# Kernel optimization log

Hardware: AMD Instinct MI355X
Metric: run time of the kernel (lower is better)

## Reference

```python
import jax, jax.numpy as jnp
import numpy as np

ALPHA, BETA, GAMMA = 1.0, 0.5, 0.25
FEATURE_DIM = 4
OHEM_RATIO = 3
K = 8  # fixed number of instance labels (0 = background)
DELTA_V, DELTA_D = 0.5, 1.5
EPS_DICE = 1e-3
EPS_IOU = 1e-6


def setup_inputs() -> dict:
    key = jax.random.key(0)
    k1, k2, k3, k4, k5 = jax.random.split(key, 5)
    B, h, w = 8, 160, 160
    H, W = 4 * h, 4 * w
    maps = jax.random.normal(k1, (B, 2 + FEATURE_DIM, h, w), jnp.float32)
    gt_texts = (jax.random.uniform(k2, (B, H, W)) > 0.5).astype(jnp.float32)
    gt_kernels = (jax.random.uniform(k3, (B, H, W)) > 0.6).astype(jnp.float32)
    training_masks = (jax.random.uniform(k4, (B, H, W)) > 0.05).astype(jnp.float32)
    gt_instance = jax.random.randint(k5, (B, H, W), 0, K).astype(jnp.int32)
    return dict(maps=maps, gt_texts=gt_texts, gt_kernels=gt_kernels,
                gt_instance=gt_instance, training_masks=training_masks)


def _up4(x):
    # F.interpolate(scale_factor=4, mode='nearest')
    return jnp.repeat(jnp.repeat(x, 4, axis=-2), 4, axis=-1)


def _dice(inp, tgt, mask):
    B = inp.shape[0]
    m = mask.reshape(B, -1)
    p = jax.nn.sigmoid(inp).reshape(B, -1) * m
    t = tgt.reshape(B, -1) * m
    a = jnp.sum(p * t, axis=1)
    b = jnp.sum(p * p, axis=1) + EPS_DICE
    c = jnp.sum(t * t, axis=1) + EPS_DICE
    return 1.0 - 2.0 * a / (b + c)  # [B]


def _ohem_single(score, gt, tm):
    pos = gt > 0.5
    pos_num = jnp.sum(pos) - jnp.sum(pos & (tm <= 0.5))
    neg = ~pos
    neg_num = jnp.minimum(pos_num * OHEM_RATIO, jnp.sum(neg))
    neg_scores = jnp.where(neg, score, -jnp.inf).ravel()
    sorted_desc = -jnp.sort(-neg_scores)
    idx = jnp.clip(neg_num - 1, 0, neg_scores.size - 1)
    thr = sorted_desc[idx]
    sel = (((score >= thr) | pos) & (tm > 0.5)).astype(tm.dtype)
    fallback = (pos_num == 0) | (neg_num == 0)
    return jnp.where(fallback, tm, sel)


def _emb_single(emb, instance, kernel, tm):
    # emb: [D,H,W]; EmbLoss v1 (agg/dis/reg), fixed K labels instead of torch.unique
    D = emb.shape[0]
    tm_b = tm > 0.5
    kn_b = kernel > 0.5
    inst = jnp.where(tm_b, instance, 0).ravel()              # instance * training_mask
    inst_k = jnp.where(kn_b & tm_b, instance, 0).ravel()     # instance * kernel
    e = emb.reshape(D, -1)                                   # [D,N]
    labels = jnp.arange(K)
    oh_k = (inst_k[None, :] == labels[:, None]).astype(e.dtype)   # [K,N]
    cnt_k = oh_k.sum(axis=1)                                  # [K]
    emb_mean = jnp.einsum('dn,kn->dk', e, oh_k) / jnp.maximum(cnt_k, 1.0)  # [D,K]
    nz = (labels != 0)
    emb_mean = emb_mean * nz[None, :].astype(e.dtype)          # torch skips lb==0 -> col0 stays 0
    present = cnt_k > 0
    valid = present & nz
    nv = jnp.sum(valid)

    # l_agg: per-pixel distance to own-instance mean
    mean_pix = emb_mean[:, inst]                               # [D,N]
    sqd = jnp.sum((e - mean_pix) ** 2, axis=0)
    dist = jnp.sqrt(jnp.maximum(sqd, 1e-12))
    val = jnp.log(jnp.maximum(dist - DELTA_V, 0.0) ** 2 + 1.0)
    oh_i = (inst[None, :] == labels[:, None]).astype(e.dtype)  # [K,N]
    cnt_i = oh_i.sum(axis=1)
    lagg_per = (oh_i @ val) / jnp.maximum(cnt_i, 1.0)          # [K]
    l_agg = jnp.sum(lagg_per * valid) / jnp.maximum(nv, 1)

    # l_dis: pairwise distances between instance means (off-diag, excl label 0)
    diff = emb_mean[:, :, None] - emb_mean[:, None, :]         # [D,K,K]
    sq = jnp.sum(diff ** 2, axis=0)
    pd = jnp.sqrt(jnp.where(sq > 0, sq, 1.0))                  # safe sqrt; diag masked below
    vdis = jnp.log(jnp.maximum(2.0 * DELTA_D - pd, 0.0) ** 2 + 1.0)
    pmask = (valid[:, None] & valid[None, :] & (~jnp.eye(K, dtype=bool))).astype(e.dtype)
    l_dis = jnp.sum(vdis * pmask) / jnp.maximum(pmask.sum(), 1.0)
    l_dis = jnp.where(nv >= 2, l_dis, 0.0)

    # l_reg over all present labels (col0 is zero -> contributes log(1)=0)
    num_instance = jnp.sum(present)
    l_reg = jnp.sum(jnp.log(jnp.linalg.norm(emb_mean, axis=0) + 1.0) * present) \
            / jnp.maximum(num_instance, 1) * 0.001

    loss = l_agg + l_dis + l_reg
    return jnp.where(nv > 0, loss, 0.0)


def reference(maps, gt_texts, gt_kernels, gt_instance, training_masks):
    p = _up4(maps)                     # [B,6,H,W]
    texts = p[:, 0]
    kernels = p[:, 1]
    embs = p[:, 2:]

    sel = jax.vmap(_ohem_single)(texts, gt_texts, training_masks)
    loss_text = _dice(texts, gt_texts, sel)

    sel_k = (jax.nn.sigmoid(texts) > 0.5).astype(texts.dtype) * training_masks
    loss_kernels = _dice(kernels, gt_kernels, sel_k)

    loss_emb = jax.vmap(_emb_single)(embs, gt_instance, gt_kernels, training_masks)

    loss = ALPHA * loss_text + BETA * loss_kernels + GAMMA * loss_emb  # [B]
    return jnp.mean(loss)  # reduction='mean'
```

## Files before the change

### kernel.cpp

```cpp
#include <hip/hip_runtime.h>
#include <math.h>

#define NB 8
#define CW 160
#define CPB (CW*CW)
#define FW 640
#define PIX (FW*FW)
#define MBLK 25

#define OFF_CNTS     0
#define OFF_CI       (NB*CPB*4)
#define OFF_CKC     (OFF_CI + NB*CPB*8)
#define OFF_PARTM   (OFF_CKC + NB*CPB*8)
#define OFF_PARTV   (OFF_PARTM + NB*MBLK*54*4)
#define WS_END      (OFF_PARTV + NB*MBLK*8*4)

__device__ __forceinline__ float wredf(float v) {
    #pragma unroll
    for (int o = 32; o; o >>= 1) v += __shfl_xor(v, o, 64);
    return v;
}
__device__ __forceinline__ int wredi(int v) {
    #pragma unroll
    for (int o = 32; o; o >>= 1) v += __shfl_xor(v, o, 64);
    return v;
}
__device__ __forceinline__ unsigned long long wredu64(unsigned long long v) {
    #pragma unroll
    for (int o = 32; o; o >>= 1) v += __shfl_xor(v, o, 64);
    return v;
}
__device__ __forceinline__ unsigned keyxf(float f) {
    unsigned bits = __float_as_uint(f);
    return (bits & 0x80000000u) ? ~bits : (bits | 0x80000000u);
}

__device__ int coscan(const int* hist, int nbins, int tid, int* s_sum) {
    int chunk = nbins >> 8;
    int base = tid * chunk;
    int s = 0;
    #pragma unroll 8
    for (int i = 0; i < chunk; i++) s += hist[base + i];
    s_sum[tid] = s;
    __syncthreads();
    #pragma unroll
    for (int off = 1; off < 256; off <<= 1) {
        int add = (tid >= off) ? s_sum[tid - off] : 0;
        __syncthreads();
        s_sum[tid] += add;
        __syncthreads();
    }
    return s_sum[255];
}
__device__ void cofind(const int* hist, int nbins, int tid,
                       const int* s_sum, int j, int* s_out) {
    int chunk = nbins >> 8;
    if (tid == 0) { s_out[0] = 0; s_out[1] = 0; }
    __syncthreads();
    int incl = s_sum[tid];
    int own = incl - ((tid > 0) ? s_sum[tid - 1] : 0);
    int excl = incl - own;
    if (j >= excl && j < incl) {
        int base = tid * chunk, cum = excl;
        for (int i = 0; i < chunk; i++) {
            int c = hist[base + i];
            if (j < cum + c) { s_out[0] = base + i; s_out[1] = j - cum; break; }
            cum += c;
        }
    }
    __syncthreads();
}
__device__ __forceinline__ int ohem_j(int pn, int N) {
    long long nn = min(3LL * (long long)pn, (long long)N);
    int j = (int)((long long)N - nn);
    if (j < 0) j = 0;
    if (j >= N) j = (N > 0) ? N - 1 : 0;
    return j;
}

__global__ __launch_bounds__(256) void k_pass1(const float* __restrict__ gt_texts,
                                               const float* __restrict__ gt_kernels,
                                               const int*   __restrict__ gt_instance,
                                               const float* __restrict__ tm,
                                               unsigned* __restrict__ cnts,
                                               unsigned long long* __restrict__ ciA,
                                               unsigned long long* __restrict__ ckA) {
    int b = blockIdx.x / 100;
    int cp = (blockIdx.x - b * 100) * 256 + threadIdx.x;
    int cy = cp / CW, cx = cp - cy * CW;
    size_t fbase = (size_t)b * PIX + (size_t)(cy * 4) * FW + cx * 4;

    float4 g[4], gk[4], m[4];
    int4 idv[4];
    #pragma unroll
    for (int r = 0; r < 4; r++) g[r]   = *reinterpret_cast<const float4*>(gt_texts   + fbase + r * FW);
    #pragma unroll
    for (int r = 0; r < 4; r++) gk[r]  = *reinterpret_cast<const float4*>(gt_kernels + fbase + r * FW);
    #pragma unroll
    for (int r = 0; r < 4; r++) m[r]   = *reinterpret_cast<const float4*>(tm         + fbase + r * FW);
    #pragma unroll
    for (int r = 0; r < 4; r++) idv[r] = *reinterpret_cast<const int4*>(gt_instance + fbase + r * FW);

    int neg = 0, c_tmb = 0, c_gt = 0, c_kb = 0;
    unsigned long long ci = 0, ck = 0;
    auto px = [&](float gg, float gkk, float mm, int id) {
        bool tmb = mm > 0.5f;
        bool gt  = gg > 0.5f;
        bool gkb = gkk > 0.5f;
        neg += !gt;
        c_tmb += tmb;
        c_gt += (gt && tmb);
        bool kb = tmb && gkb;
        c_kb += kb;
        ci += 1ull << ((tmb ? id : 0) * 8);
        ck += 1ull << ((kb ? id : 0) * 8);
    };
    #pragma unroll
    for (int r = 0; r < 4; r++) {
        px(g[r].x, gk[r].x, m[r].x, idv[r].x);
        px(g[r].y, gk[r].y, m[r].y, idv[r].y);
        px(g[r].z, gk[r].z, m[r].z, idv[r].z);
        px(g[r].w, gk[r].w, m[r].w, idv[r].w);
    }
    int gidx = b * CPB + cp;
    cnts[gidx] = (unsigned)c_tmb | ((unsigned)c_gt << 8) | ((unsigned)c_kb << 16) | ((unsigned)neg << 24);
    ciA[gidx] = ci;
    ckA[gidx] = ck;
}

__global__ __launch_bounds__(256) void k_main_c(const float* __restrict__ maps,
                                                const unsigned* __restrict__ cnts,
                                                const unsigned long long* __restrict__ ciA,
                                                const unsigned long long* __restrict__ ckA,
                                                float* __restrict__ partM) {
    int b = blockIdx.x / MBLK;
    int blk = blockIdx.x - b * MBLK;
    int tid = threadIdx.x;
    const float* tex = maps + (size_t)b * 6 * CPB;
    const unsigned* cn = cnts + b * CPB;

    __shared__ int h[2048];
    __shared__ int s_sum[256];
    __shared__ int s_out[2];
    __shared__ int s_pos[4];

    for (int i = tid; i < 2048; i += 256) h[i] = 0;
    __syncthreads();
    int posSum = 0;
    for (int it = 0; it < 25; it++) {
        int i0 = (it * 256 + tid) * 4;
        float4 t4 = *reinterpret_cast<const float4*>(tex + i0);
        uint4  c4 = *reinterpret_cast<const uint4*>(cn + i0);
        float tv[4] = {t4.x, t4.y, t4.z, t4.w};
        unsigned cv[4] = {c4.x, c4.y, c4.z, c4.w};
        #pragma unroll
        for (int j = 0; j < 4; j++) {
            posSum += (int)((cv[j] >> 8) & 255);
            int w = (int)(cv[j] >> 24);
            if (w) atomicAdd(&h[keyxf(tv[j]) >> 21], w);
        }
    }
    posSum = wredi(posSum);
    if ((tid & 63) == 0) s_pos[tid >> 6] = posSum;
    __syncthreads();
    int pn = s_pos[0] + s_pos[1] + s_pos[2] + s_pos[3];
    int N = coscan(h, 2048, tid, s_sum);
    long long nn = min(3LL * (long long)pn, (long long)N);
    int fb = (pn == 0 || nn == 0) ? 1 : 0;
    int j0 = ohem_j(pn, N);
    cofind(h, 2048, tid, s_sum, j0, s_out);
    int d0 = s_out[0], j1 = s_out[1];
    __syncthreads();

    for (int i = tid; i < 2048; i += 256) h[i] = 0;
    __syncthreads();
    for (int it = 0; it < 25; it++) {
        int i0 = (it * 256 + tid) * 4;
        float4 t4 = *reinterpret_cast<const float4*>(tex + i0);
        uint4  c4 = *reinterpret_cast<const uint4*>(cn + i0);
        float tv[4] = {t4.x, t4.y, t4.z, t4.w};
        unsigned cv[4] = {c4.x, c4.y, c4.z, c4.w};
        #pragma unroll
        for (int j = 0; j < 4; j++) {
            int w = (int)(cv[j] >> 24);
            if (!w) continue;
            unsigned key = keyxf(tv[j]);
            if ((int)(key >> 21) == d0) atomicAdd(&h[(key >> 10) & 0x7FF], w);
        }
    }
    __syncthreads();
    coscan(h, 2048, tid, s_sum);
    cofind(h, 2048, tid, s_sum, j1, s_out);
    int d1 = s_out[0], j2 = s_out[1];
    unsigned pref = ((unsigned)d0 << 11) | (unsigned)d1;
    __syncthreads();

    for (int i = tid; i < 1024; i += 256) h[i] = 0;
    __syncthreads();
    for (int it = 0; it < 25; it++) {
        int i0 = (it * 256 + tid) * 4;
        float4 t4 = *reinterpret_cast<const float4*>(tex + i0);
        uint4  c4 = *reinterpret_cast<const uint4*>(cn + i0);
        float tv[4] = {t4.x, t4.y, t4.z, t4.w};
        unsigned cv[4] = {c4.x, c4.y, c4.z, c4.w};
        #pragma unroll
        for (int j = 0; j < 4; j++) {
            int w = (int)(cv[j] >> 24);
            if (!w) continue;
            unsigned key = keyxf(tv[j]);
            if ((key >> 10) == pref) atomicAdd(&h[key & 0x3FF], w);
        }
    }
    __syncthreads();
    coscan(h, 1024, tid, s_sum);
    cofind(h, 1024, tid, s_sum, j2, s_out);
    unsigned key = ((unsigned)d0 << 21) | ((unsigned)d1 << 10) | (unsigned)s_out[0];
    unsigned tbits = (key & 0x80000000u) ? (key & 0x7FFFFFFFu) : ~key;
    float thr = __uint_as_float(tbits);

    int p0 = (blk * 256 + tid) * 4;
    const float* mb = maps + (size_t)b * 6 * CPB;
    float txa[4], kna[4], e0a[4], e1a[4], e2a[4], e3a[4];
    *reinterpret_cast<float4*>(txa) = *reinterpret_cast<const float4*>(mb + p0);
    *reinterpret_cast<float4*>(kna) = *reinterpret_cast<const float4*>(mb + CPB + p0);
    *reinterpret_cast<float4*>(e0a) = *reinterpret_cast<const float4*>(mb + 2 * CPB + p0);
    *reinterpret_cast<float4*>(e1a) = *reinterpret_cast<const float4*>(mb + 3 * CPB + p0);
    *reinterpret_cast<float4*>(e2a) = *reinterpret_cast<const float4*>(mb + 4 * CPB + p0);
    *reinterpret_cast<float4*>(e3a) = *reinterpret_cast<const float4*>(mb + 5 * CPB + p0);
    unsigned ca[4];
    *reinterpret_cast<uint4*>(ca) = *reinterpret_cast<const uint4*>(cnts + b * CPB + p0);
    unsigned long long cia[4], cka[4];
    *reinterpret_cast<ulonglong2*>(cia)     = *reinterpret_cast<const ulonglong2*>(ciA + b * CPB + p0);
    *reinterpret_cast<ulonglong2*>(cia + 2) = *reinterpret_cast<const ulonglong2*>(ciA + b * CPB + p0 + 2);
    *reinterpret_cast<ulonglong2*>(cka)     = *reinterpret_cast<const ulonglong2*>(ckA + b * CPB + p0);
    *reinterpret_cast<ulonglong2*>(cka + 2) = *reinterpret_cast<const ulonglong2*>(ckA + b * CPB + p0 + 2);

    float at = 0.f, bt = 0.f, ct = 0.f, ak = 0.f, bk = 0.f, ckd = 0.f;
    unsigned long long ciS = 0, ckS = 0;
    float se[4][8];
    #pragma unroll
    for (int d = 0; d < 4; d++)
        #pragma unroll
        for (int k = 0; k < 8; k++) se[d][k] = 0.f;

    #pragma unroll
    for (int j = 0; j < 4; j++) {
        float tx = txa[j], kn = kna[j];
        unsigned c = ca[j];
        float c_tmb = (float)(c & 255);
        float c_gt  = (float)((c >> 8) & 255);
        float c_kb  = (float)((c >> 16) & 255);
        float sig_t = 1.f / (1.f + expf(-tx));
        float sig_k = 1.f / (1.f + expf(-kn));
        bool sge = (tx >= thr);
        bool skp = (tx > 0.0f);
        float n_sel = fb ? c_tmb : (sge ? c_tmb : c_gt);
        float n_selk = skp ? c_tmb : 0.f;
        float n_selk_g = skp ? c_kb : 0.f;
        at += sig_t * c_gt;
        bt += sig_t * sig_t * n_sel;
        ct += c_gt;
        ak += sig_k * n_selk_g;
        bk += sig_k * sig_k * n_selk;
        ckd += n_selk_g;
        ciS += cia[j];
        unsigned long long ck = cka[j];
        ckS += ck;
        #pragma unroll
        for (int k = 1; k < 8; k++) {
            float fc = (float)((ck >> (8 * k)) & 255);
            se[0][k] += e0a[j] * fc;
            se[1][k] += e1a[j] * fc;
            se[2][k] += e2a[j] * fc;
            se[3][k] += e3a[j] * fc;
        }
    }

    at = wredf(at); bt = wredf(bt); ct = wredf(ct);
    ak = wredf(ak); bk = wredf(bk); ckd = wredf(ckd);
    const unsigned long long M = 0x00FF00FF00FF00FFull;
    unsigned long long ci0 = wredu64(ciS & M);
    unsigned long long ci1 = wredu64((ciS >> 8) & M);
    unsigned long long ck0 = wredu64(ckS & M);
    unsigned long long ck1 = wredu64((ckS >> 8) & M);
    #pragma unroll
    for (int d = 0; d < 4; d++)
        #pragma unroll
        for (int k = 1; k < 8; k++) se[d][k] = wredf(se[d][k]);

    __shared__ float sh[4][54];
    int w = tid >> 6;
    if ((tid & 63) == 0) {
        sh[w][0] = at; sh[w][1] = bt; sh[w][2] = ct;
        sh[w][3] = ak; sh[w][4] = bk; sh[w][5] = ckd;
        #pragma unroll
        for (int q = 0; q < 4; q++) {
            sh[w][6 + 2 * q]      = (float)((ck0 >> (16 * q)) & 0xFFFF);
            sh[w][6 + 2 * q + 1]  = (float)((ck1 >> (16 * q)) & 0xFFFF);
            sh[w][14 + 2 * q]     = (float)((ci0 >> (16 * q)) & 0xFFFF);
            sh[w][14 + 2 * q + 1] = (float)((ci1 >> (16 * q)) & 0xFFFF);
        }
        #pragma unroll
        for (int d = 0; d < 4; d++) {
            sh[w][22 + d * 8] = 0.f;
            #pragma unroll
            for (int k = 1; k < 8; k++) sh[w][22 + d * 8 + k] = se[d][k];
        }
    }
    __syncthreads();
    if (tid < 54)
        partM[(size_t)(b * MBLK + blk) * 54 + tid] =
            sh[0][tid] + sh[1][tid] + sh[2][tid] + sh[3][tid];
}

__global__ __launch_bounds__(256) void k_val_c(const float* __restrict__ maps,
                                               const unsigned long long* __restrict__ ciA,
                                               const float* __restrict__ partM,
                                               float* __restrict__ partV) {
    int b = blockIdx.x / MBLK;
    int blk = blockIdx.x - b * MBLK;
    int tid = threadIdx.x;
    int p0 = (blk * 256 + tid) * 4;
    const float* mb = maps + (size_t)b * 6 * CPB;

    float e0a[4], e1a[4], e2a[4], e3a[4];
    *reinterpret_cast<float4*>(e0a) = *reinterpret_cast<const float4*>(mb + 2 * CPB + p0);
    *reinterpret_cast<float4*>(e1a) = *reinterpret_cast<const float4*>(mb + 3 * CPB + p0);
    *reinterpret_cast<float4*>(e2a) = *reinterpret_cast<const float4*>(mb + 4 * CPB + p0);
    *reinterpret_cast<float4*>(e3a) = *reinterpret_cast<const float4*>(mb + 5 * CPB + p0);
    unsigned long long cia[4];
    *reinterpret_cast<ulonglong2*>(cia)     = *reinterpret_cast<const ulonglong2*>(ciA + b * CPB + p0);
    *reinterpret_cast<ulonglong2*>(cia + 2) = *reinterpret_cast<const ulonglong2*>(ciA + b * CPB + p0 + 2);

    __shared__ float A54[54];
    __shared__ float shm[32];
    __shared__ float shv[8];
    if (tid < 54) {
        float s = 0.f;
        #pragma unroll 5
        for (int j = 0; j < MBLK; j++) s += partM[(size_t)(b * MBLK + j) * 54 + tid];
        A54[tid] = s;
    }
    __syncthreads();
    if (tid < 32) {
        int k = tid & 7;
        shm[tid] = (k == 0) ? 0.f : A54[22 + tid] / fmaxf(A54[6 + k], 1.f);
    }
    if (tid < 8) shv[tid] = (tid != 0 && A54[6 + tid] > 0.f) ? 1.f : 0.f;
    __syncthreads();

    float sv[8];
    #pragma unroll
    for (int k = 0; k < 8; k++) sv[k] = 0.f;
    #pragma unroll
    for (int j = 0; j < 4; j++) {
        unsigned long long ci = cia[j];
        #pragma unroll
        for (int k = 1; k < 8; k++) {
            int c = (int)((ci >> (8 * k)) & 255);
            if (c && shv[k] > 0.5f) {
                float d0 = e0a[j] - shm[k], d1 = e1a[j] - shm[8 + k];
                float d2 = e2a[j] - shm[16 + k], d3 = e3a[j] - shm[24 + k];
                float sq = d0 * d0 + d1 * d1 + d2 * d2 + d3 * d3;
                float dist = sqrtf(fmaxf(sq, 1e-12f));
                float t = fmaxf(dist - 0.5f, 0.f);
                sv[k] += logf(t * t + 1.f) * (float)c;
            }
        }
    }
    #pragma unroll
    for (int k = 1; k < 8; k++) sv[k] = wredf(sv[k]);
    __shared__ float shp[4][8];
    int w = tid >> 6;
    if ((tid & 63) == 0) {
        shp[w][0] = 0.f;
        #pragma unroll
        for (int k = 1; k < 8; k++) shp[w][k] = sv[k];
    }
    __syncthreads();
    if (tid < 8)
        partV[(size_t)(b * MBLK + blk) * 8 + tid] =
            shp[0][tid] + shp[1][tid] + shp[2][tid] + shp[3][tid];
}

__global__ __launch_bounds__(64) void k_final(const float* __restrict__ partM,
                                              const float* __restrict__ partV,
                                              float* __restrict__ out) {
    int tid = threadIdx.x;
    __shared__ float AM[NB][54];
    __shared__ float SV[NB][8];
    __shared__ float tot[NB];
    for (int i = tid; i < NB * 54; i += 64) {
        int b = i / 54, c = i - b * 54;
        float s = 0.f;
        for (int j = 0; j < MBLK; j++) s += partM[(size_t)(b * MBLK + j) * 54 + c];
        AM[b][c] = s;
    }
    {
        int b = tid >> 3, k = tid & 7;
        float s = 0.f;
        for (int j = 0; j < MBLK; j++) s += partV[(size_t)(b * MBLK + j) * 8 + k];
        SV[b][k] = s;
    }
    __syncthreads();
    if (tid < NB) {
        int b = tid;
        const float* A = AM[b];
        float ltext = 1.f - 2.f * A[0] / (A[1] + A[2] + 0.002f);
        float lkern = 1.f - 2.f * A[3] / (A[4] + A[5] + 0.002f);
        float m[4][8];
        float valid[8];
        int nv = 0, ninst = 0;
        #pragma unroll
        for (int k = 0; k < 8; k++) {
            float c = A[6 + k];
            float inv = 1.f / fmaxf(c, 1.f);
            #pragma unroll
            for (int d = 0; d < 4; d++) m[d][k] = (k == 0) ? 0.f : A[22 + d * 8 + k] * inv;
            int pres = (c > 0.f);
            ninst += pres;
            int v = pres && (k != 0);
            nv += v;
            valid[k] = (float)v;
        }
        float s = 0.f;
        for (int i = 1; i < 8; i++) {
            if (valid[i] < 0.5f) continue;
            for (int j = 1; j < 8; j++) {
                if (j == i || valid[j] < 0.5f) continue;
                float sq = 0.f;
                #pragma unroll
                for (int d = 0; d < 4; d++) { float df = m[d][i] - m[d][j]; sq += df * df; }
                float pd = sqrtf(sq > 0.f ? sq : 1.f);
                float t = fmaxf(3.f - pd, 0.f);
                s += logf(t * t + 1.f);
            }
        }
        float pairs = (float)(nv * nv - nv);
        float l_dis = (nv >= 2) ? s / fmaxf(pairs, 1.f) : 0.f;
        float s2 = 0.f;
        for (int k = 0; k < 8; k++) {
            if (A[6 + k] > 0.f) {
                float n2 = 0.f;
                #pragma unroll
                for (int d = 0; d < 4; d++) n2 += m[d][k] * m[d][k];
                s2 += logf(sqrtf(n2) + 1.f);
            }
        }
        float l_reg = s2 / fmaxf((float)ninst, 1.f) * 0.001f;
        float lagg = 0.f;
        #pragma unroll
        for (int k = 0; k < 8; k++)
            lagg += valid[k] * (SV[b][k] / fmaxf(A[14 + k], 1.f));
        lagg /= fmaxf((float)nv, 1.f);
        float le = (nv > 0) ? (lagg + l_dis + l_reg) : 0.f;
        tot[b] = ltext + 0.5f * lkern + 0.25f * le;
    }
    __syncthreads();
    if (tid == 0) {
        float t = 0.f;
        for (int b = 0; b < NB; b++) t += tot[b];
        out[0] = t / (float)NB;
    }
}

extern "C" void kernel_launch(void* const* d_in, const int* in_sizes, int n_in,
                              void* d_out, int out_size, void* d_ws, size_t ws_size,
                              hipStream_t stream) {
    const float* maps        = (const float*)d_in[0];
    const float* gt_texts    = (const float*)d_in[1];
    const float* gt_kernels  = (const float*)d_in[2];
    const int*   gt_instance = (const int*)d_in[3];
    const float* tm          = (const float*)d_in[4];
    char* ws = (char*)d_ws;
    unsigned* cnts  = (unsigned*)(ws + OFF_CNTS);
    unsigned long long* ciA = (unsigned long long*)(ws + OFF_CI);
    unsigned long long* ckA = (unsigned long long*)(ws + OFF_CKC);
    float* partM    = (float*)(ws + OFF_PARTM);
    float* partV    = (float*)(ws + OFF_PARTV);

    k_pass1<<<NB * 100, 256, 0, stream>>>(gt_texts, gt_kernels, gt_instance, tm,
                                          cnts, ciA, ckA);
    k_main_c<<<NB * MBLK, 256, 0, stream>>>(maps, cnts, ciA, ckA, partM);
    k_val_c<<<NB * MBLK, 256, 0, stream>>>(maps, ciA, partM, partV);
    k_final<<<1, 64, 0, stream>>>(partM, partV, (float*)d_out);
}
```

Baseline: 165.3 us.

## Split OHEM threshold selection into a per-batch kernel with wave-shuffle scan

Before, each of the 25 k_main_c blocks per image recomputed the same three-pass radix-select OHEM threshold over the whole image. That selection now runs once per image in a new 1024-thread kernel k_sel, which stores the threshold and fallback flag in workspace for k_main_c to read. The block prefix scan is rebuilt around wave shuffles, replacing the log-step barrier loop. This removes the redundant histogram passes but adds a kernel launch, and only 8 blocks run during selection, so the device is poorly occupied in that phase.

```diff
diff --git a/kernel.cpp b/kernel.cpp
--- a/kernel.cpp
+++ b/kernel.cpp
@@ -13,7 +13,9 @@
 #define OFF_CKC     (OFF_CI + NB*CPB*8)
 #define OFF_PARTM   (OFF_CKC + NB*CPB*8)
 #define OFF_PARTV   (OFF_PARTM + NB*MBLK*54*4)
-#define WS_END      (OFF_PARTV + NB*MBLK*8*4)
+#define OFF_THR     (OFF_PARTV + NB*MBLK*8*4)
+#define OFF_FB      (OFF_THR + NB*4)
+#define WS_END      (OFF_FB + NB*4)
 
 __device__ __forceinline__ float wredf(float v) {
     #pragma unroll
@@ -35,31 +37,36 @@
     return (bits & 0x80000000u) ? ~bits : (bits | 0x80000000u);
 }
 
-__device__ int coscan(const int* hist, int nbins, int tid, int* s_sum) {
-    int chunk = nbins >> 8;
+__device__ int coscan(const int* hist, int nbins, int tid, int* s_sum, int* s_w) {
+    int chunk = nbins >> 10;
     int base = tid * chunk;
     int s = 0;
-    #pragma unroll 8
+    #pragma unroll 2
     for (int i = 0; i < chunk; i++) s += hist[base + i];
-    s_sum[tid] = s;
-    __syncthreads();
-    #pragma unroll
-    for (int off = 1; off < 256; off <<= 1) {
-        int add = (tid >= off) ? s_sum[tid - off] : 0;
-        __syncthreads();
-        s_sum[tid] += add;
-        __syncthreads();
-    }
-    return s_sum[255];
+    int lane = tid & 63, wid = tid >> 6;
+    int inc = s;
+    #pragma unroll
+    for (int off = 1; off < 64; off <<= 1) {
+        int u = __shfl_up(inc, off, 64);
+        if (lane >= off) inc += u;
+    }
+    if (lane == 63) s_w[wid] = inc;
+    __syncthreads();
+    int wpre = 0;
+    #pragma unroll
+    for (int i = 0; i < 15; i++) wpre += (i < wid) ? s_w[i] : 0;
+    int incl = inc + wpre;
+    s_sum[tid] = incl;
+    __syncthreads();
+    return s_sum[1023];
 }
 __device__ void cofind(const int* hist, int nbins, int tid,
                        const int* s_sum, int j, int* s_out) {
-    int chunk = nbins >> 8;
+    int chunk = nbins >> 10;
     if (tid == 0) { s_out[0] = 0; s_out[1] = 0; }
     __syncthreads();
     int incl = s_sum[tid];
-    int own = incl - ((tid > 0) ? s_sum[tid - 1] : 0);
-    int excl = incl - own;
+    int excl = (tid > 0) ? s_sum[tid - 1] : 0;
     if (j >= excl && j < incl) {
         int base = tid * chunk, cum = excl;
         for (int i = 0; i < chunk; i++) {
@@ -128,43 +135,45 @@
     ckA[gidx] = ck;
 }
 
-__global__ __launch_bounds__(256) void k_main_c(const float* __restrict__ maps,
-                                                const unsigned* __restrict__ cnts,
-                                                const unsigned long long* __restrict__ ciA,
-                                                const unsigned long long* __restrict__ ckA,
-                                                float* __restrict__ partM) {
-    int b = blockIdx.x / MBLK;
-    int blk = blockIdx.x - b * MBLK;
-    int tid = threadIdx.x;
+__global__ __launch_bounds__(1024) void k_sel(const float* __restrict__ maps,
+                                              const unsigned* __restrict__ cnts,
+                                              float* __restrict__ thrArr,
+                                              int* __restrict__ fbArr) {
+    int b = blockIdx.x, tid = threadIdx.x;
     const float* tex = maps + (size_t)b * 6 * CPB;
     const unsigned* cn = cnts + b * CPB;
-
     __shared__ int h[2048];
-    __shared__ int s_sum[256];
+    __shared__ int s_sum[1024];
+    __shared__ int s_w[16];
+    __shared__ int s_pos[16];
     __shared__ int s_out[2];
-    __shared__ int s_pos[4];
-
-    for (int i = tid; i < 2048; i += 256) h[i] = 0;
+
+    for (int i = tid; i < 2048; i += 1024) h[i] = 0;
     __syncthreads();
     int posSum = 0;
-    for (int it = 0; it < 25; it++) {
-        int i0 = (it * 256 + tid) * 4;
-        float4 t4 = *reinterpret_cast<const float4*>(tex + i0);
-        uint4  c4 = *reinterpret_cast<const uint4*>(cn + i0);
-        float tv[4] = {t4.x, t4.y, t4.z, t4.w};
-        unsigned cv[4] = {c4.x, c4.y, c4.z, c4.w};
-        #pragma unroll
-        for (int j = 0; j < 4; j++) {
-            posSum += (int)((cv[j] >> 8) & 255);
-            int w = (int)(cv[j] >> 24);
-            if (w) atomicAdd(&h[keyxf(tv[j]) >> 21], w);
+    #pragma unroll
+    for (int it = 0; it < 7; it++) {
+        int i0 = (it * 1024 + tid) * 4;
+        if (i0 < CPB) {
+            float4 t4 = *reinterpret_cast<const float4*>(tex + i0);
+            uint4  c4 = *reinterpret_cast<const uint4*>(cn + i0);
+            float tv[4] = {t4.x, t4.y, t4.z, t4.w};
+            unsigned cv[4] = {c4.x, c4.y, c4.z, c4.w};
+            #pragma unroll
+            for (int j = 0; j < 4; j++) {
+                posSum += (int)((cv[j] >> 8) & 255);
+                int w = (int)(cv[j] >> 24);
+                if (w) atomicAdd(&h[keyxf(tv[j]) >> 21], w);
+            }
         }
     }
     posSum = wredi(posSum);
     if ((tid & 63) == 0) s_pos[tid >> 6] = posSum;
     __syncthreads();
-    int pn = s_pos[0] + s_pos[1] + s_pos[2] + s_pos[3];
-    int N = coscan(h, 2048, tid, s_sum);
+    int pn = 0;
+    #pragma unroll
+    for (int i = 0; i < 16; i++) pn += s_pos[i];
+    int N = coscan(h, 2048, tid, s_sum, s_w);
     long long nn = min(3LL * (long long)pn, (long long)N);
     int fb = (pn == 0 || nn == 0) ? 1 : 0;
     int j0 = ohem_j(pn, N);
@@ -172,54 +181,75 @@
     int d0 = s_out[0], j1 = s_out[1];
     __syncthreads();
 
-    for (int i = tid; i < 2048; i += 256) h[i] = 0;
-    __syncthreads();
-    for (int it = 0; it < 25; it++) {
-        int i0 = (it * 256 + tid) * 4;
-        float4 t4 = *reinterpret_cast<const float4*>(tex + i0);
-        uint4  c4 = *reinterpret_cast<const uint4*>(cn + i0);
-        float tv[4] = {t4.x, t4.y, t4.z, t4.w};
-        unsigned cv[4] = {c4.x, c4.y, c4.z, c4.w};
-        #pragma unroll
-        for (int j = 0; j < 4; j++) {
-            int w = (int)(cv[j] >> 24);
-            if (!w) continue;
-            unsigned key = keyxf(tv[j]);
-            if ((int)(key >> 21) == d0) atomicAdd(&h[(key >> 10) & 0x7FF], w);
-        }
-    }
-    __syncthreads();
-    coscan(h, 2048, tid, s_sum);
+    for (int i = tid; i < 2048; i += 1024) h[i] = 0;
+    __syncthreads();
+    #pragma unroll
+    for (int it = 0; it < 7; it++) {
+        int i0 = (it * 1024 + tid) * 4;
+        if (i0 < CPB) {
+            float4 t4 = *reinterpret_cast<const float4*>(tex + i0);
+            uint4  c4 = *reinterpret_cast<const uint4*>(cn + i0);
+            float tv[4] = {t4.x, t4.y, t4.z, t4.w};
+            unsigned cv[4] = {c4.x, c4.y, c4.z, c4.w};
+            #pragma unroll
+            for (int j = 0; j < 4; j++) {
+                int w = (int)(cv[j] >> 24);
+                if (!w) continue;
+                unsigned key = keyxf(tv[j]);
+                if ((int)(key >> 21) == d0) atomicAdd(&h[(key >> 10) & 0x7FF], w);
+            }
+        }
+    }
+    __syncthreads();
+    coscan(h, 2048, tid, s_sum, s_w);
     cofind(h, 2048, tid, s_sum, j1, s_out);
     int d1 = s_out[0], j2 = s_out[1];
     unsigned pref = ((unsigned)d0 << 11) | (unsigned)d1;
     __syncthreads();
 
-    for (int i = tid; i < 1024; i += 256) h[i] = 0;
-    __syncthreads();
-    for (int it = 0; it < 25; it++) {
-        int i0 = (it * 256 + tid) * 4;
-        float4 t4 = *reinterpret_cast<const float4*>(tex + i0);
-        uint4  c4 = *reinterpret_cast<const uint4*>(cn + i0);
-        float tv[4] = {t4.x, t4.y, t4.z, t4.w};
-        unsigned cv[4] = {c4.x, c4.y, c4.z, c4.w};
-        #pragma unroll
-        for (int j = 0; j < 4; j++) {
-            int w = (int)(cv[j] >> 24);
-            if (!w) continue;
-            unsigned key = keyxf(tv[j]);
-            if ((key >> 10) == pref) atomicAdd(&h[key & 0x3FF], w);
-        }
-    }
-    __syncthreads();
-    coscan(h, 1024, tid, s_sum);
+    if (tid < 1024) h[tid] = 0;
+    __syncthreads();
+    #pragma unroll
+    for (int it = 0; it < 7; it++) {
+        int i0 = (it * 1024 + tid) * 4;
+        if (i0 < CPB) {
+            float4 t4 = *reinterpret_cast<const float4*>(tex + i0);
+            uint4  c4 = *reinterpret_cast<const uint4*>(cn + i0);
+            float tv[4] = {t4.x, t4.y, t4.z, t4.w};
+            unsigned cv[4] = {c4.x, c4.y, c4.z, c4.w};
+            #pragma unroll
+            for (int j = 0; j < 4; j++) {
+                int w = (int)(cv[j] >> 24);
+                if (!w) continue;
+                unsigned key = keyxf(tv[j]);
+                if ((key >> 10) == pref) atomicAdd(&h[key & 0x3FF], w);
+            }
+        }
+    }
+    __syncthreads();
+    coscan(h, 1024, tid, s_sum, s_w);
     cofind(h, 1024, tid, s_sum, j2, s_out);
-    unsigned key = ((unsigned)d0 << 21) | ((unsigned)d1 << 10) | (unsigned)s_out[0];
-    unsigned tbits = (key & 0x80000000u) ? (key & 0x7FFFFFFFu) : ~key;
-    float thr = __uint_as_float(tbits);
-
+    if (tid == 0) {
+        unsigned key = ((unsigned)d0 << 21) | ((unsigned)d1 << 10) | (unsigned)s_out[0];
+        unsigned bits = (key & 0x80000000u) ? (key & 0x7FFFFFFFu) : ~key;
+        thrArr[b] = __uint_as_float(bits);
+        fbArr[b] = fb;
+    }
+}
+
+__global__ __launch_bounds__(256) void k_main_c(const float* __restrict__ maps,
+                                                const unsigned* __restrict__ cnts,
+                                                const unsigned long long* __restrict__ ciA,
+                                                const unsigned long long* __restrict__ ckA,
+                                                const float* __restrict__ thrArr,
+                                                const int* __restrict__ fbArr,
+                                                float* __restrict__ partM) {
+    int b = blockIdx.x / MBLK;
+    int blk = blockIdx.x - b * MBLK;
+    int tid = threadIdx.x;
     int p0 = (blk * 256 + tid) * 4;
     const float* mb = maps + (size_t)b * 6 * CPB;
+
     float txa[4], kna[4], e0a[4], e1a[4], e2a[4], e3a[4];
     *reinterpret_cast<float4*>(txa) = *reinterpret_cast<const float4*>(mb + p0);
     *reinterpret_cast<float4*>(kna) = *reinterpret_cast<const float4*>(mb + CPB + p0);
@@ -234,6 +264,8 @@
     *reinterpret_cast<ulonglong2*>(cia + 2) = *reinterpret_cast<const ulonglong2*>(ciA + b * CPB + p0 + 2);
     *reinterpret_cast<ulonglong2*>(cka)     = *reinterpret_cast<const ulonglong2*>(ckA + b * CPB + p0);
     *reinterpret_cast<ulonglong2*>(cka + 2) = *reinterpret_cast<const ulonglong2*>(ckA + b * CPB + p0 + 2);
+    float thr = thrArr[b];
+    int fb = fbArr[b];
 
     float at = 0.f, bt = 0.f, ct = 0.f, ak = 0.f, bk = 0.f, ckd = 0.f;
     unsigned long long ciS = 0, ckS = 0;
@@ -478,10 +510,13 @@
     unsigned long long* ckA = (unsigned long long*)(ws + OFF_CKC);
     float* partM    = (float*)(ws + OFF_PARTM);
     float* partV    = (float*)(ws + OFF_PARTV);
+    float* thrArr   = (float*)(ws + OFF_THR);
+    int*   fbArr    = (int*)(ws + OFF_FB);
 
     k_pass1<<<NB * 100, 256, 0, stream>>>(gt_texts, gt_kernels, gt_instance, tm,
                                           cnts, ciA, ckA);
-    k_main_c<<<NB * MBLK, 256, 0, stream>>>(maps, cnts, ciA, ckA, partM);
+    k_sel<<<NB, 1024, 0, stream>>>(maps, cnts, thrArr, fbArr);
+    k_main_c<<<NB * MBLK, 256, 0, stream>>>(maps, cnts, ciA, ckA, thrArr, fbArr, partM);
     k_val_c<<<NB * MBLK, 256, 0, stream>>>(maps, ciA, partM, partV);
     k_final<<<1, 64, 0, stream>>>(partM, partV, (float*)d_out);
 }
```

Result: faster. 140.1 us (-15.2%).
